# Kernel optimization log

Hardware: AMD Instinct MI355X
Metric: run time of the kernel (lower is better)

Reference implementation:

```python
import jax, jax.numpy as jnp
import numpy as np

# SMPL kinematic tree, first 22 joints (root has parent -1)
PARENTS = [-1, 0, 0, 0, 1, 2, 3, 4, 5, 6, 7, 8, 9, 9, 9, 12, 13, 14, 16, 17, 18, 19]
B, L, J = 64, 2048, 22


def axis_angle_to_matrix(aa):
    """aa: (..., 3) axis-angle -> (..., 3, 3) rotation matrix (Rodrigues)."""
    sq = jnp.sum(aa * aa, axis=-1, keepdims=True)
    angle = jnp.sqrt(sq + 1e-12)
    axis = aa / angle
    x, y, z = axis[..., 0], axis[..., 1], axis[..., 2]
    ang = angle[..., 0]
    c, s = jnp.cos(ang), jnp.sin(ang)
    t = 1.0 - c
    R = jnp.stack([
        t * x * x + c,     t * x * y - s * z, t * x * z + s * y,
        t * x * y + s * z, t * y * y + c,     t * y * z - s * x,
        t * x * z - s * y, t * y * z + s * x, t * z * z + c,
    ], axis=-1)
    return R.reshape(aa.shape[:-1] + (3, 3))


def get_TRS(rotmat, pos):
    """rotmat (...,3,3), pos (...,3) -> homogeneous (...,4,4)."""
    top = jnp.concatenate([rotmat, pos[..., :, None]], axis=-1)  # (...,3,4)
    bottom = jnp.broadcast_to(
        jnp.array([0.0, 0.0, 0.0, 1.0], rotmat.dtype), top.shape[:-2] + (1, 4))
    return jnp.concatenate([top, bottom], axis=-2)


def forward_kinematics(mat, parents):
    """mat: (B,L,J,4,4) local transforms -> global transforms via parent chain."""
    out = [mat[:, :, 0]]
    for j in range(1, mat.shape[2]):
        out.append(out[parents[j]] @ mat[:, :, j])
    return jnp.stack(out, axis=2)


def setup_inputs() -> dict:
    key = jax.random.key(0)
    ks = jax.random.split(key, 6)
    return {
        "body_pose": 0.3 * jax.random.normal(ks[0], (B, L, 63), jnp.float32),
        "betas": jax.random.normal(ks[1], (B, L, 10), jnp.float32),
        "global_orient": 0.3 * jax.random.normal(ks[2], (B, L, 3), jnp.float32),
        "transl": jax.random.normal(ks[3], (B, L, 3), jnp.float32),
        "J_template": jax.random.normal(ks[4], (J, 3), jnp.float32),
        "J_shapedirs": 0.01 * jax.random.normal(ks[5], (J, 3, 10), jnp.float32),
    }


def reference(body_pose, betas, global_orient, transl, J_template, J_shapedirs):
    Bm, Lm = body_pose.shape[:2]
    # (B,L,22,3) axis-angle: global orient + 21 body joints
    aa = jnp.concatenate([global_orient, body_pose], axis=-1).reshape(Bm, Lm, -1, 3)
    rotmat = axis_angle_to_matrix(aa)                                  # (B,L,22,3,3)
    skeleton = J_template[None, None] + jnp.einsum('blk,jck->bljc', betas, J_shapedirs)
    # local offsets: child - parent, root keeps its own position (+ transl)
    parent_idx = jnp.array([0] + PARENTS[1:])
    local = skeleton - skeleton[:, :, parent_idx]
    local = local.at[:, :, 0].set(skeleton[:, :, 0] + transl)
    mat = get_TRS(rotmat, local)                                       # (B,L,22,4,4)
    fk_mat = forward_kinematics(mat, PARENTS)                          # (B,L,22,4,4)
    joints = fk_mat[..., :3, 3]                                        # (B,L,22,3)
    return joints
```

## Files before the change

### kernel.cpp

```cpp
#include <hip/hip_runtime.h>

#define NT  128
#define WSZ 64
#define NJ  22

struct X9 { float r[9]; float t[3]; };

__device__ __forceinline__ void rodrigues(float ax, float ay, float az, float* R) {
    float sq   = ax*ax + ay*ay + az*az + 1e-12f;
    float rinv = rsqrtf(sq);
    float ang  = sq * rinv;
    float s, c;
    __sincosf(ang, &s, &c);
    float x = ax*rinv, y = ay*rinv, z = az*rinv;
    float t = 1.0f - c;
    R[0] = t*x*x + c;   R[1] = t*x*y - s*z; R[2] = t*x*z + s*y;
    R[3] = t*x*y + s*z; R[4] = t*y*y + c;   R[5] = t*y*z - s*x;
    R[6] = t*x*z - s*y; R[7] = t*y*z + s*x; R[8] = t*z*z + c;
}

__device__ __forceinline__ void local_pos(int j, const float* bt,
                                          const float4* LD4, float* lt) {
    #pragma unroll
    for (int c = 0; c < 3; ++c) {
        const float4 a0 = LD4[(j*3 + c)*3 + 0];
        const float4 a1 = LD4[(j*3 + c)*3 + 1];
        const float4 a2 = LD4[(j*3 + c)*3 + 2];
        float v = a2.z;
        v = fmaf(bt[0], a0.x, v); v = fmaf(bt[1], a0.y, v);
        v = fmaf(bt[2], a0.z, v); v = fmaf(bt[3], a0.w, v);
        v = fmaf(bt[4], a1.x, v); v = fmaf(bt[5], a1.y, v);
        v = fmaf(bt[6], a1.z, v); v = fmaf(bt[7], a1.w, v);
        v = fmaf(bt[8], a2.x, v); v = fmaf(bt[9], a2.y, v);
        lt[c] = v;
    }
}

template<int J>
__device__ __forceinline__ X9 step(const X9& gp, const float* aa, const float* bt,
                                   const float4* LD4, float* s_o) {
    float R[9];
    rodrigues(aa[(J-1)*3 + 0], aa[(J-1)*3 + 1], aa[(J-1)*3 + 2], R);
    float lt[3];
    local_pos(J, bt, LD4, lt);
    X9 g;
    #pragma unroll
    for (int r = 0; r < 3; ++r) {
        #pragma unroll
        for (int c = 0; c < 3; ++c)
            g.r[r*3+c] = fmaf(gp.r[r*3+0], R[c],
                         fmaf(gp.r[r*3+1], R[3+c],
                              gp.r[r*3+2] * R[6+c]));
        g.t[r] = fmaf(gp.r[r*3+0], lt[0],
                 fmaf(gp.r[r*3+1], lt[1],
                 fmaf(gp.r[r*3+2], lt[2], gp.t[r])));
    }
    s_o[J*3+0] = g.t[0]; s_o[J*3+1] = g.t[1]; s_o[J*3+2] = g.t[2];
    return g;
}

__global__ __launch_bounds__(NT)
__attribute__((amdgpu_waves_per_eu(2, 2)))
void fk_joints_kernel(
    const float* __restrict__ body_pose,
    const float* __restrict__ betas,
    const float* __restrict__ global_orient,
    const float* __restrict__ transl,
    const float* __restrict__ J_template,
    const float* __restrict__ J_shapedirs,
    float* __restrict__ out)
{
    __shared__ float  s_buf[NT*66];
    __shared__ float4 s_LD4[NJ*3*3];

    const int  tid  = threadIdx.x;
    const int  lane = tid & (WSZ-1);
    const int  wid  = tid >> 6;
    const long long sw = (long long)blockIdx.x * NT + (long long)wid * WSZ;
    const long long s  = sw + lane;

    const float gox = global_orient[s*3 + 0];
    const float goy = global_orient[s*3 + 1];
    const float goz = global_orient[s*3 + 2];
    const float trx = transl[s*3 + 0];
    const float try_ = transl[s*3 + 1];
    const float trz = transl[s*3 + 2];
    float bt[10];
    {
        const float2* b2 = reinterpret_cast<const float2*>(betas + s*10);
        #pragma unroll
        for (int k = 0; k < 5; ++k) {
            float2 v = b2[k];
            bt[2*k+0] = v.x; bt[2*k+1] = v.y;
        }
    }

    float* myb = s_buf + wid * (WSZ*66);
    {
        const float4* src = reinterpret_cast<const float4*>(body_pose + sw*63);
        float4* dst = reinterpret_cast<float4*>(myb);
        #pragma unroll
        for (int i = lane; i < WSZ*63/4; i += WSZ) dst[i] = src[i];
    }

    const int P[NJ] = {0,0,0,0,1,2,3,4,5,6,7,8,9,9,9,12,13,14,16,17,18,19};
    float* s_LD = reinterpret_cast<float*>(s_LD4);
    for (int i = lane; i < NJ*3; i += WSZ) {
        int j = i/3, c = i - j*3;
        float v = J_template[i];
        if (j) v -= J_template[P[j]*3 + c];
        s_LD[i*12 + 10] = v;
        s_LD[i*12 + 11] = 0.0f;
    }
    for (int i = lane; i < NJ*30; i += WSZ) {
        int jc = i/10, k = i - jc*10;
        int j = jc/3,  c = jc - j*3;
        float v = J_shapedirs[i];
        if (j) v -= J_shapedirs[(P[j]*3 + c)*10 + k];
        s_LD[jc*12 + k] = v;
    }
    __builtin_amdgcn_wave_barrier();

    float aa[63];
    #pragma unroll
    for (int k = 0; k < 63; ++k) aa[k] = myb[lane*63 + k];
    __builtin_amdgcn_wave_barrier();

    float* s_o = myb + lane*66;

    X9 g0;
    rodrigues(gox, goy, goz, g0.r);
    {
        float lt0[3];
        local_pos(0, bt, s_LD4, lt0);
        g0.t[0] = lt0[0] + trx;
        g0.t[1] = lt0[1] + try_;
        g0.t[2] = lt0[2] + trz;
        s_o[0] = g0.t[0]; s_o[1] = g0.t[1]; s_o[2] = g0.t[2];
    }

    X9 g;
    g = step<1 >(g0, aa, bt, s_LD4, s_o);
    g = step<4 >(g,  aa, bt, s_LD4, s_o);
    g = step<7 >(g,  aa, bt, s_LD4, s_o);
    g = step<10>(g,  aa, bt, s_LD4, s_o);
    g = step<2 >(g0, aa, bt, s_LD4, s_o);
    g = step<5 >(g,  aa, bt, s_LD4, s_o);
    g = step<8 >(g,  aa, bt, s_LD4, s_o);
    g = step<11>(g,  aa, bt, s_LD4, s_o);
    g = step<3 >(g0, aa, bt, s_LD4, s_o);
    g = step<6 >(g,  aa, bt, s_LD4, s_o);
    X9 g9 = step<9>(g, aa, bt, s_LD4, s_o);
    g = step<12>(g9, aa, bt, s_LD4, s_o);
    g = step<15>(g,  aa, bt, s_LD4, s_o);
    g = step<13>(g9, aa, bt, s_LD4, s_o);
    g = step<16>(g,  aa, bt, s_LD4, s_o);
    g = step<18>(g,  aa, bt, s_LD4, s_o);
    g = step<20>(g,  aa, bt, s_LD4, s_o);
    g = step<14>(g9, aa, bt, s_LD4, s_o);
    g = step<17>(g,  aa, bt, s_LD4, s_o);
    g = step<19>(g,  aa, bt, s_LD4, s_o);
    g = step<21>(g,  aa, bt, s_LD4, s_o);

    __builtin_amdgcn_wave_barrier();

    {
        const float4* src = reinterpret_cast<const float4*>(myb);
        float4* dst = reinterpret_cast<float4*>(out + sw * (NJ*3));
        #pragma unroll
        for (int i = lane; i < WSZ*66/4; i += WSZ) dst[i] = src[i];
    }
}

extern "C" void kernel_launch(void* const* d_in, const int* in_sizes, int n_in,
                              void* d_out, int out_size, void* d_ws, size_t ws_size,
                              hipStream_t stream) {
    const float* body_pose     = (const float*)d_in[0];
    const float* betas         = (const float*)d_in[1];
    const float* global_orient = (const float*)d_in[2];
    const float* transl        = (const float*)d_in[3];
    const float* J_template    = (const float*)d_in[4];
    const float* J_shapedirs   = (const float*)d_in[5];
    float* out = (float*)d_out;

    const int S = in_sizes[0] / 63;
    const int blocks = S / NT;

    hipLaunchKernelGGL(fk_joints_kernel, dim3(blocks), dim3(NT), 0, stream,
                       body_pose, betas, global_orient, transl,
                       J_template, J_shapedirs, out);
}
```

Before: 31.36 us.

## Split each sample's kinematic chain across two lanes for parallel FK

Each wave now processes 32 samples, and two lanes share one sample's kinematic tree. Each lane walks half the joint chains in a fixed 11-step schedule, and joint 9's transform is passed between the pair with shuffles. This halves per-thread register use and serial depth and doubles thread count (256 threads per block, 4 blocks per CU hint). The cost is duplicated root and beta work, extra selects, and a shuffle. Each thread also now loads only 33 pose values instead of 63.

```diff
diff --git a/kernel.cpp b/kernel.cpp
--- a/kernel.cpp
+++ b/kernel.cpp
@@ -1,10 +1,16 @@
 #include <hip/hip_runtime.h>
 
-#define NT  128
-#define WSZ 64
-#define NJ  22
-
-struct X9 { float r[9]; float t[3]; };
+#define NT   256
+#define WSZ  64
+#define SPW  32
+#define NJ   22
+
+__constant__ __device__ const int dummy_unused = 0;
+
+constexpr int cJ0[11] = {3,6,9, 2,5,8,11, 13,16,18,20};
+constexpr int cS0[11] = {1,0,0, 1,0,0,0,  2, 0, 0, 0};
+constexpr int cJ1[11] = {1,4,7,10, 12,15, 14,17,19,21, 12};
+constexpr int cS1[11] = {1,0,0,0,  2, 0,  2, 0, 0, 0,  2};
 
 __device__ __forceinline__ void rodrigues(float ax, float ay, float az, float* R) {
     float sq   = ax*ax + ay*ay + az*az + 1e-12f;
@@ -19,8 +25,8 @@
     R[6] = t*x*z - s*y; R[7] = t*y*z + s*x; R[8] = t*z*z + c;
 }
 
-__device__ __forceinline__ void local_pos(int j, const float* bt,
-                                          const float4* LD4, float* lt) {
+__device__ __forceinline__ void local_pos_rt(int j, const float* bt,
+                                             const float4* LD4, float* lt) {
     #pragma unroll
     for (int c = 0; c < 3; ++c) {
         const float4 a0 = LD4[(j*3 + c)*3 + 0];
@@ -36,32 +42,52 @@
     }
 }
 
-template<int J>
-__device__ __forceinline__ X9 step(const X9& gp, const float* aa, const float* bt,
-                                   const float4* LD4, float* s_o) {
+template<int S>
+__device__ __forceinline__ const float* psel(const float* g, const float* g0, const float* g9s) {
+    if constexpr (S == 0) return g;
+    else if constexpr (S == 1) return g0;
+    else return g9s;
+}
+
+template<int T>
+__device__ __forceinline__ void step2(float* g, const float* g0, const float* g9s,
+                                      int h, const float* aa, const float* bt,
+                                      const float4* LD4, float* s_o ) {
+    constexpr int J0 = cJ0[T], J1 = cJ1[T], S0 = cS0[T], S1 = cS1[T];
+    float gp[12];
+    if constexpr (S0 == S1) {
+        const float* a = psel<S0>(g, g0, g9s);
+        #pragma unroll
+        for (int i = 0; i < 12; ++i) gp[i] = a[i];
+    } else {
+        const float* a = psel<S0>(g, g0, g9s);
+        const float* b = psel<S1>(g, g0, g9s);
+        #pragma unroll
+        for (int i = 0; i < 12; ++i) gp[i] = h ? b[i] : a[i];
+    }
+    const int j = h ? J1 : J0;
     float R[9];
-    rodrigues(aa[(J-1)*3 + 0], aa[(J-1)*3 + 1], aa[(J-1)*3 + 2], R);
+    rodrigues(aa[T*3 + 0], aa[T*3 + 1], aa[T*3 + 2], R);
     float lt[3];
-    local_pos(J, bt, LD4, lt);
-    X9 g;
+    local_pos_rt(j, bt, LD4, lt);
+    float gn[12];
     #pragma unroll
     for (int r = 0; r < 3; ++r) {
         #pragma unroll
         for (int c = 0; c < 3; ++c)
-            g.r[r*3+c] = fmaf(gp.r[r*3+0], R[c],
-                         fmaf(gp.r[r*3+1], R[3+c],
-                              gp.r[r*3+2] * R[6+c]));
-        g.t[r] = fmaf(gp.r[r*3+0], lt[0],
-                 fmaf(gp.r[r*3+1], lt[1],
-                 fmaf(gp.r[r*3+2], lt[2], gp.t[r])));
-    }
-    s_o[J*3+0] = g.t[0]; s_o[J*3+1] = g.t[1]; s_o[J*3+2] = g.t[2];
-    return g;
-}
-
-__global__ __launch_bounds__(NT)
-__attribute__((amdgpu_waves_per_eu(2, 2)))
-void fk_joints_kernel(
+            gn[r*3+c] = fmaf(gp[r*3+0], R[c],
+                        fmaf(gp[r*3+1], R[3+c],
+                             gp[r*3+2] * R[6+c]));
+        gn[9+r] = fmaf(gp[r*3+0], lt[0],
+                  fmaf(gp[r*3+1], lt[1],
+                  fmaf(gp[r*3+2], lt[2], gp[9+r])));
+    }
+    s_o[j*3+0] = gn[9]; s_o[j*3+1] = gn[10]; s_o[j*3+2] = gn[11];
+    #pragma unroll
+    for (int i = 0; i < 12; ++i) g[i] = gn[i];
+}
+
+__global__ __launch_bounds__(NT, 4) void fk_joints_kernel(
     const float* __restrict__ body_pose,
     const float* __restrict__ betas,
     const float* __restrict__ global_orient,
@@ -70,14 +96,16 @@
     const float* __restrict__ J_shapedirs,
     float* __restrict__ out)
 {
-    __shared__ float  s_buf[NT*66];
+    __shared__ float  s_buf[4 * SPW * 66];
     __shared__ float4 s_LD4[NJ*3*3];
 
     const int  tid  = threadIdx.x;
     const int  lane = tid & (WSZ-1);
     const int  wid  = tid >> 6;
-    const long long sw = (long long)blockIdx.x * NT + (long long)wid * WSZ;
-    const long long s  = sw + lane;
+    const int  samp = lane >> 1;
+    const int  h    = lane & 1;
+    const long long sw = (long long)blockIdx.x * (4*SPW) + (long long)wid * SPW;
+    const long long s  = sw + samp;
 
     const float gox = global_orient[s*3 + 0];
     const float goy = global_orient[s*3 + 1];
@@ -95,12 +123,12 @@
         }
     }
 
-    float* myb = s_buf + wid * (WSZ*66);
+    float* myb = s_buf + wid * (SPW*66);
     {
         const float4* src = reinterpret_cast<const float4*>(body_pose + sw*63);
         float4* dst = reinterpret_cast<float4*>(myb);
         #pragma unroll
-        for (int i = lane; i < WSZ*63/4; i += WSZ) dst[i] = src[i];
+        for (int i = lane; i < SPW*63/4; i += WSZ) dst[i] = src[i];
     }
 
     const int P[NJ] = {0,0,0,0,1,2,3,4,5,6,7,8,9,9,9,12,13,14,16,17,18,19};
@@ -121,54 +149,60 @@
     }
     __builtin_amdgcn_wave_barrier();
 
-    float aa[63];
-    #pragma unroll
-    for (int k = 0; k < 63; ++k) aa[k] = myb[lane*63 + k];
+    float aa[33];
+    {
+        const float* mypose = myb + samp*63;
+        #pragma unroll
+        for (int t = 0; t < 11; ++t) {
+            const int off = (h ? (cJ1[t]-1) : (cJ0[t]-1)) * 3;
+            aa[t*3+0] = mypose[off+0];
+            aa[t*3+1] = mypose[off+1];
+            aa[t*3+2] = mypose[off+2];
+        }
+    }
+
+    float g0[12];
+    rodrigues(gox, goy, goz, g0);
+    {
+        float lt0[3];
+        local_pos_rt(0, bt, s_LD4, lt0);
+        g0[9]  = lt0[0] + trx;
+        g0[10] = lt0[1] + try_;
+        g0[11] = lt0[2] + trz;
+    }
     __builtin_amdgcn_wave_barrier();
 
-    float* s_o = myb + lane*66;
-
-    X9 g0;
-    rodrigues(gox, goy, goz, g0.r);
-    {
-        float lt0[3];
-        local_pos(0, bt, s_LD4, lt0);
-        g0.t[0] = lt0[0] + trx;
-        g0.t[1] = lt0[1] + try_;
-        g0.t[2] = lt0[2] + trz;
-        s_o[0] = g0.t[0]; s_o[1] = g0.t[1]; s_o[2] = g0.t[2];
-    }
-
-    X9 g;
-    g = step<1 >(g0, aa, bt, s_LD4, s_o);
-    g = step<4 >(g,  aa, bt, s_LD4, s_o);
-    g = step<7 >(g,  aa, bt, s_LD4, s_o);
-    g = step<10>(g,  aa, bt, s_LD4, s_o);
-    g = step<2 >(g0, aa, bt, s_LD4, s_o);
-    g = step<5 >(g,  aa, bt, s_LD4, s_o);
-    g = step<8 >(g,  aa, bt, s_LD4, s_o);
-    g = step<11>(g,  aa, bt, s_LD4, s_o);
-    g = step<3 >(g0, aa, bt, s_LD4, s_o);
-    g = step<6 >(g,  aa, bt, s_LD4, s_o);
-    X9 g9 = step<9>(g, aa, bt, s_LD4, s_o);
-    g = step<12>(g9, aa, bt, s_LD4, s_o);
-    g = step<15>(g,  aa, bt, s_LD4, s_o);
-    g = step<13>(g9, aa, bt, s_LD4, s_o);
-    g = step<16>(g,  aa, bt, s_LD4, s_o);
-    g = step<18>(g,  aa, bt, s_LD4, s_o);
-    g = step<20>(g,  aa, bt, s_LD4, s_o);
-    g = step<14>(g9, aa, bt, s_LD4, s_o);
-    g = step<17>(g,  aa, bt, s_LD4, s_o);
-    g = step<19>(g,  aa, bt, s_LD4, s_o);
-    g = step<21>(g,  aa, bt, s_LD4, s_o);
+    float* s_o = myb + samp*66;
+    s_o[0] = g0[9]; s_o[1] = g0[10]; s_o[2] = g0[11];
+
+    float g[12];
+    float g9s[12];
+    #pragma unroll
+    for (int i = 0; i < 12; ++i) g9s[i] = 0.0f;
+
+    step2<0>(g, g0, g9s, h, aa, bt, s_LD4, s_o);
+    step2<1>(g, g0, g9s, h, aa, bt, s_LD4, s_o);
+    step2<2>(g, g0, g9s, h, aa, bt, s_LD4, s_o);
+    {
+        const int pairlane = lane & ~1;
+        #pragma unroll
+        for (int i = 0; i < 12; ++i) g9s[i] = __shfl(g[i], pairlane, WSZ);
+    }
+    step2<3>(g, g0, g9s, h, aa, bt, s_LD4, s_o);
+    step2<4>(g, g0, g9s, h, aa, bt, s_LD4, s_o);
+    step2<5>(g, g0, g9s, h, aa, bt, s_LD4, s_o);
+    step2<6>(g, g0, g9s, h, aa, bt, s_LD4, s_o);
+    step2<7>(g, g0, g9s, h, aa, bt, s_LD4, s_o);
+    step2<8>(g, g0, g9s, h, aa, bt, s_LD4, s_o);
+    step2<9>(g, g0, g9s, h, aa, bt, s_LD4, s_o);
+    step2<10>(g, g0, g9s, h, aa, bt, s_LD4, s_o);
 
     __builtin_amdgcn_wave_barrier();
 
     {
         const float4* src = reinterpret_cast<const float4*>(myb);
         float4* dst = reinterpret_cast<float4*>(out + sw * (NJ*3));
-        #pragma unroll
-        for (int i = lane; i < WSZ*66/4; i += WSZ) dst[i] = src[i];
+        for (int i = lane; i < SPW*66/4; i += WSZ) dst[i] = src[i];
     }
 }
 
@@ -184,7 +218,7 @@
     float* out = (float*)d_out;
 
     const int S = in_sizes[0] / 63;
-    const int blocks = S / NT;
+    const int blocks = S / (4*SPW);
 
     hipLaunchKernelGGL(fk_joints_kernel, dim3(blocks), dim3(NT), 0, stream,
                        body_pose, betas, global_orient, transl,
```

Result: slower. 49.52 us (+57.9%).

## Compute skeleton per thread in registers and reuse pose LDS in place

Applied to the files above, without the earlier changes.

Drops the shared-memory table of parent-differenced shape directions. Each thread now regresses its full 22-joint skeleton from betas directly, reading J_shapedirs and J_template as uniform global loads, then subtracts parent positions. Instead of copying all 63 pose values into registers, each step reads its axis-angle from LDS and overwrites the same slots with the joint position. The root goes to a separate small array, and output is gathered with index arithmetic. It also removes the waves_per_eu attribute and shrinks LDS. The cost is more per-thread FMAs (skeleton regression plus subtraction), many scalar constant loads, and a divide/modulo gather in the store loop.

```diff
diff --git a/kernel.cpp b/kernel.cpp
--- a/kernel.cpp
+++ b/kernel.cpp
@@ -3,6 +3,8 @@
 #define NT  128
 #define WSZ 64
 #define NJ  22
+
+constexpr int PARENT[NJ] = {0,0,0,0,1,2,3,4,5,6,7,8,9,9,9,12,13,14,16,17,18,19};
 
 struct X9 { float r[9]; float t[3]; };
 
@@ -19,30 +21,11 @@
     R[6] = t*x*z - s*y; R[7] = t*y*z + s*x; R[8] = t*z*z + c;
 }
 
-__device__ __forceinline__ void local_pos(int j, const float* bt,
-                                          const float4* LD4, float* lt) {
-    #pragma unroll
-    for (int c = 0; c < 3; ++c) {
-        const float4 a0 = LD4[(j*3 + c)*3 + 0];
-        const float4 a1 = LD4[(j*3 + c)*3 + 1];
-        const float4 a2 = LD4[(j*3 + c)*3 + 2];
-        float v = a2.z;
-        v = fmaf(bt[0], a0.x, v); v = fmaf(bt[1], a0.y, v);
-        v = fmaf(bt[2], a0.z, v); v = fmaf(bt[3], a0.w, v);
-        v = fmaf(bt[4], a1.x, v); v = fmaf(bt[5], a1.y, v);
-        v = fmaf(bt[6], a1.z, v); v = fmaf(bt[7], a1.w, v);
-        v = fmaf(bt[8], a2.x, v); v = fmaf(bt[9], a2.y, v);
-        lt[c] = v;
-    }
-}
-
 template<int J>
-__device__ __forceinline__ X9 step(const X9& gp, const float* aa, const float* bt,
-                                   const float4* LD4, float* s_o) {
+__device__ __forceinline__ X9 step(const X9& gp, float* pp, const float* sk) {
     float R[9];
-    rodrigues(aa[(J-1)*3 + 0], aa[(J-1)*3 + 1], aa[(J-1)*3 + 2], R);
-    float lt[3];
-    local_pos(J, bt, LD4, lt);
+    rodrigues(pp[(J-1)*3 + 0], pp[(J-1)*3 + 1], pp[(J-1)*3 + 2], R);
+    const float l0 = sk[J*3+0], l1 = sk[J*3+1], l2 = sk[J*3+2];
     X9 g;
     #pragma unroll
     for (int r = 0; r < 3; ++r) {
@@ -51,17 +34,15 @@
             g.r[r*3+c] = fmaf(gp.r[r*3+0], R[c],
                          fmaf(gp.r[r*3+1], R[3+c],
                               gp.r[r*3+2] * R[6+c]));
-        g.t[r] = fmaf(gp.r[r*3+0], lt[0],
-                 fmaf(gp.r[r*3+1], lt[1],
-                 fmaf(gp.r[r*3+2], lt[2], gp.t[r])));
+        g.t[r] = fmaf(gp.r[r*3+0], l0,
+                 fmaf(gp.r[r*3+1], l1,
+                 fmaf(gp.r[r*3+2], l2, gp.t[r])));
     }
-    s_o[J*3+0] = g.t[0]; s_o[J*3+1] = g.t[1]; s_o[J*3+2] = g.t[2];
+    pp[(J-1)*3+0] = g.t[0]; pp[(J-1)*3+1] = g.t[1]; pp[(J-1)*3+2] = g.t[2];
     return g;
 }
 
-__global__ __launch_bounds__(NT)
-__attribute__((amdgpu_waves_per_eu(2, 2)))
-void fk_joints_kernel(
+__global__ __launch_bounds__(NT) void fk_joints_kernel(
     const float* __restrict__ body_pose,
     const float* __restrict__ betas,
     const float* __restrict__ global_orient,
@@ -70,14 +51,22 @@
     const float* __restrict__ J_shapedirs,
     float* __restrict__ out)
 {
-    __shared__ float  s_buf[NT*66];
-    __shared__ float4 s_LD4[NJ*3*3];
+    __shared__ float s_buf[NT*63];
+    __shared__ float s_root[NT*3];
 
     const int  tid  = threadIdx.x;
     const int  lane = tid & (WSZ-1);
     const int  wid  = tid >> 6;
     const long long sw = (long long)blockIdx.x * NT + (long long)wid * WSZ;
     const long long s  = sw + lane;
+
+    float* myb = s_buf + wid * (WSZ*63);
+
+    {
+        const float4* src = reinterpret_cast<const float4*>(body_pose + sw*63);
+        float4* dst = reinterpret_cast<float4*>(myb);
+        for (int i = lane; i < WSZ*63/4; i += WSZ) dst[i] = src[i];
+    }
 
     const float gox = global_orient[s*3 + 0];
     const float goy = global_orient[s*3 + 1];
@@ -95,80 +84,75 @@
         }
     }
 
-    float* myb = s_buf + wid * (WSZ*66);
-    {
-        const float4* src = reinterpret_cast<const float4*>(body_pose + sw*63);
-        float4* dst = reinterpret_cast<float4*>(myb);
+    float sk[NJ*3];
+    #pragma unroll
+    for (int j = 0; j < NJ; ++j) {
         #pragma unroll
-        for (int i = lane; i < WSZ*63/4; i += WSZ) dst[i] = src[i];
+        for (int c = 0; c < 3; ++c) {
+            float v = J_template[j*3 + c];
+            #pragma unroll
+            for (int k = 0; k < 10; ++k)
+                v = fmaf(bt[k], J_shapedirs[(j*3 + c)*10 + k], v);
+            sk[j*3 + c] = v;
+        }
     }
-
-    const int P[NJ] = {0,0,0,0,1,2,3,4,5,6,7,8,9,9,9,12,13,14,16,17,18,19};
-    float* s_LD = reinterpret_cast<float*>(s_LD4);
-    for (int i = lane; i < NJ*3; i += WSZ) {
-        int j = i/3, c = i - j*3;
-        float v = J_template[i];
-        if (j) v -= J_template[P[j]*3 + c];
-        s_LD[i*12 + 10] = v;
-        s_LD[i*12 + 11] = 0.0f;
+    #pragma unroll
+    for (int j = NJ-1; j >= 1; --j) {
+        #pragma unroll
+        for (int c = 0; c < 3; ++c) sk[j*3 + c] -= sk[PARENT[j]*3 + c];
     }
-    for (int i = lane; i < NJ*30; i += WSZ) {
-        int jc = i/10, k = i - jc*10;
-        int j = jc/3,  c = jc - j*3;
-        float v = J_shapedirs[i];
-        if (j) v -= J_shapedirs[(P[j]*3 + c)*10 + k];
-        s_LD[jc*12 + k] = v;
-    }
-    __builtin_amdgcn_wave_barrier();
-
-    float aa[63];
-    #pragma unroll
-    for (int k = 0; k < 63; ++k) aa[k] = myb[lane*63 + k];
-    __builtin_amdgcn_wave_barrier();
-
-    float* s_o = myb + lane*66;
 
     X9 g0;
     rodrigues(gox, goy, goz, g0.r);
-    {
-        float lt0[3];
-        local_pos(0, bt, s_LD4, lt0);
-        g0.t[0] = lt0[0] + trx;
-        g0.t[1] = lt0[1] + try_;
-        g0.t[2] = lt0[2] + trz;
-        s_o[0] = g0.t[0]; s_o[1] = g0.t[1]; s_o[2] = g0.t[2];
-    }
+    g0.t[0] = sk[0] + trx;
+    g0.t[1] = sk[1] + try_;
+    g0.t[2] = sk[2] + trz;
+    s_root[tid*3+0] = g0.t[0]; s_root[tid*3+1] = g0.t[1]; s_root[tid*3+2] = g0.t[2];
+
+    __builtin_amdgcn_wave_barrier();
+
+    float* pp = myb + lane*63;
 
     X9 g;
-    g = step<1 >(g0, aa, bt, s_LD4, s_o);
-    g = step<4 >(g,  aa, bt, s_LD4, s_o);
-    g = step<7 >(g,  aa, bt, s_LD4, s_o);
-    g = step<10>(g,  aa, bt, s_LD4, s_o);
-    g = step<2 >(g0, aa, bt, s_LD4, s_o);
-    g = step<5 >(g,  aa, bt, s_LD4, s_o);
-    g = step<8 >(g,  aa, bt, s_LD4, s_o);
-    g = step<11>(g,  aa, bt, s_LD4, s_o);
-    g = step<3 >(g0, aa, bt, s_LD4, s_o);
-    g = step<6 >(g,  aa, bt, s_LD4, s_o);
-    X9 g9 = step<9>(g, aa, bt, s_LD4, s_o);
-    g = step<12>(g9, aa, bt, s_LD4, s_o);
-    g = step<15>(g,  aa, bt, s_LD4, s_o);
-    g = step<13>(g9, aa, bt, s_LD4, s_o);
-    g = step<16>(g,  aa, bt, s_LD4, s_o);
-    g = step<18>(g,  aa, bt, s_LD4, s_o);
-    g = step<20>(g,  aa, bt, s_LD4, s_o);
-    g = step<14>(g9, aa, bt, s_LD4, s_o);
-    g = step<17>(g,  aa, bt, s_LD4, s_o);
-    g = step<19>(g,  aa, bt, s_LD4, s_o);
-    g = step<21>(g,  aa, bt, s_LD4, s_o);
+    g = step<1 >(g0, pp, sk);
+    g = step<4 >(g,  pp, sk);
+    g = step<7 >(g,  pp, sk);
+    g = step<10>(g,  pp, sk);
+    g = step<2 >(g0, pp, sk);
+    g = step<5 >(g,  pp, sk);
+    g = step<8 >(g,  pp, sk);
+    g = step<11>(g,  pp, sk);
+    g = step<3 >(g0, pp, sk);
+    g = step<6 >(g,  pp, sk);
+    X9 g9 = step<9>(g, pp, sk);
+    g = step<12>(g9, pp, sk);
+    g = step<15>(g,  pp, sk);
+    g = step<13>(g9, pp, sk);
+    g = step<16>(g,  pp, sk);
+    g = step<18>(g,  pp, sk);
+    g = step<20>(g,  pp, sk);
+    g = step<14>(g9, pp, sk);
+    g = step<17>(g,  pp, sk);
+    g = step<19>(g,  pp, sk);
+    g = step<21>(g,  pp, sk);
 
     __builtin_amdgcn_wave_barrier();
 
     {
-        const float4* src = reinterpret_cast<const float4*>(myb);
+        const float* s_rootw = s_root + wid * (WSZ*3);
         float4* dst = reinterpret_cast<float4*>(out + sw * (NJ*3));
-        #pragma unroll
-        for (int i = lane; i < WSZ*66/4; i += WSZ) dst[i] = src[i];
+        for (int i = lane; i < WSZ*66/4; i += WSZ) {
+            const int f0 = i*4;
+            float v[4];
+            #pragma unroll
+            for (int q = 0; q < 4; ++q) {
+                int f = f0 + q;
+                int sm = f / 66;
+                int r = f - sm*66;
+                v[q] = (r < 3) ? s_rootw[sm*3 + r] : myb[sm*63 + (r - 3)];
+            }
+            dst[i] = make_float4(v[0], v[1], v[2], v[3]);
+        }
     }
 }
 
```

Result: slower. 44.67 us (median of 2 runs) (+42.4%).

## Replace unrolled FK chain with table-driven loop to cut register pressure

Applied to the files above, without the earlier changes.

Replaces the fully unrolled per-joint template chain, and the 63-float register array of axis-angles, with a runtime loop driven by a constant-memory schedule table. Each step reads its pose from LDS and writes the joint position back in place. The root position goes to a separate LDS array and the output is assembled with per-element index math. Shared memory per block shrinks and the waves_per_eu cap is removed, aiming for lower VGPR use and higher occupancy. The cost is loop overhead, branching on the schedule code, integer divides in the store loop and LDS reads in the critical path.

```diff
diff --git a/kernel.cpp b/kernel.cpp
--- a/kernel.cpp
+++ b/kernel.cpp
@@ -4,7 +4,15 @@
 #define WSZ 64
 #define NJ  22
 
-struct X9 { float r[9]; float t[3]; };
+__constant__ int c_code[21] = {
+    1|(1<<8), 4, 7, 10,
+    2|(1<<8), 5, 8, 11,
+    3|(1<<8), 6, 9,
+    12|(2<<8), 15,
+    13|(2<<8), 16, 18, 20,
+    14|(2<<8), 17, 19, 21
+};
+__constant__ int c_par[NJ] = {0,0,0,0,1,2,3,4,5,6,7,8,9,9,9,12,13,14,16,17,18,19};
 
 __device__ __forceinline__ void rodrigues(float ax, float ay, float az, float* R) {
     float sq   = ax*ax + ay*ay + az*az + 1e-12f;
@@ -19,8 +27,8 @@
     R[6] = t*x*z - s*y; R[7] = t*y*z + s*x; R[8] = t*z*z + c;
 }
 
-__device__ __forceinline__ void local_pos(int j, const float* bt,
-                                          const float4* LD4, float* lt) {
+__device__ __forceinline__ void local_pos_rt(int j, const float* bt,
+                                             const float4* LD4, float* lt) {
     #pragma unroll
     for (int c = 0; c < 3; ++c) {
         const float4 a0 = LD4[(j*3 + c)*3 + 0];
@@ -36,32 +44,7 @@
     }
 }
 
-template<int J>
-__device__ __forceinline__ X9 step(const X9& gp, const float* aa, const float* bt,
-                                   const float4* LD4, float* s_o) {
-    float R[9];
-    rodrigues(aa[(J-1)*3 + 0], aa[(J-1)*3 + 1], aa[(J-1)*3 + 2], R);
-    float lt[3];
-    local_pos(J, bt, LD4, lt);
-    X9 g;
-    #pragma unroll
-    for (int r = 0; r < 3; ++r) {
-        #pragma unroll
-        for (int c = 0; c < 3; ++c)
-            g.r[r*3+c] = fmaf(gp.r[r*3+0], R[c],
-                         fmaf(gp.r[r*3+1], R[3+c],
-                              gp.r[r*3+2] * R[6+c]));
-        g.t[r] = fmaf(gp.r[r*3+0], lt[0],
-                 fmaf(gp.r[r*3+1], lt[1],
-                 fmaf(gp.r[r*3+2], lt[2], gp.t[r])));
-    }
-    s_o[J*3+0] = g.t[0]; s_o[J*3+1] = g.t[1]; s_o[J*3+2] = g.t[2];
-    return g;
-}
-
-__global__ __launch_bounds__(NT)
-__attribute__((amdgpu_waves_per_eu(2, 2)))
-void fk_joints_kernel(
+__global__ __launch_bounds__(NT) void fk_joints_kernel(
     const float* __restrict__ body_pose,
     const float* __restrict__ betas,
     const float* __restrict__ global_orient,
@@ -70,7 +53,8 @@
     const float* __restrict__ J_shapedirs,
     float* __restrict__ out)
 {
-    __shared__ float  s_buf[NT*66];
+    __shared__ float  s_buf[NT*63];
+    __shared__ float  s_root[NT*3];
     __shared__ float4 s_LD4[NJ*3*3];
 
     const int  tid  = threadIdx.x;
@@ -78,6 +62,15 @@
     const int  wid  = tid >> 6;
     const long long sw = (long long)blockIdx.x * NT + (long long)wid * WSZ;
     const long long s  = sw + lane;
+
+    float* myb = s_buf + wid * (WSZ*63);
+
+    {
+        const float4* src = reinterpret_cast<const float4*>(body_pose + sw*63);
+        float4* dst = reinterpret_cast<float4*>(myb);
+        #pragma unroll 1
+        for (int i = lane; i < WSZ*63/4; i += WSZ) dst[i] = src[i];
+    }
 
     const float gox = global_orient[s*3 + 0];
     const float goy = global_orient[s*3 + 1];
@@ -95,80 +88,94 @@
         }
     }
 
-    float* myb = s_buf + wid * (WSZ*66);
-    {
-        const float4* src = reinterpret_cast<const float4*>(body_pose + sw*63);
-        float4* dst = reinterpret_cast<float4*>(myb);
-        #pragma unroll
-        for (int i = lane; i < WSZ*63/4; i += WSZ) dst[i] = src[i];
-    }
-
-    const int P[NJ] = {0,0,0,0,1,2,3,4,5,6,7,8,9,9,9,12,13,14,16,17,18,19};
     float* s_LD = reinterpret_cast<float*>(s_LD4);
+    #pragma unroll 1
     for (int i = lane; i < NJ*3; i += WSZ) {
         int j = i/3, c = i - j*3;
         float v = J_template[i];
-        if (j) v -= J_template[P[j]*3 + c];
+        if (j) v -= J_template[c_par[j]*3 + c];
         s_LD[i*12 + 10] = v;
         s_LD[i*12 + 11] = 0.0f;
     }
+    #pragma unroll 1
     for (int i = lane; i < NJ*30; i += WSZ) {
         int jc = i/10, k = i - jc*10;
         int j = jc/3,  c = jc - j*3;
         float v = J_shapedirs[i];
-        if (j) v -= J_shapedirs[(P[j]*3 + c)*10 + k];
+        if (j) v -= J_shapedirs[(c_par[j]*3 + c)*10 + k];
         s_LD[jc*12 + k] = v;
     }
     __builtin_amdgcn_wave_barrier();
 
-    float aa[63];
-    #pragma unroll
-    for (int k = 0; k < 63; ++k) aa[k] = myb[lane*63 + k];
-    __builtin_amdgcn_wave_barrier();
-
-    float* s_o = myb + lane*66;
-
-    X9 g0;
-    rodrigues(gox, goy, goz, g0.r);
+    float g[12], g0r[12], g9r[12];
+    rodrigues(gox, goy, goz, g0r);
     {
         float lt0[3];
-        local_pos(0, bt, s_LD4, lt0);
-        g0.t[0] = lt0[0] + trx;
-        g0.t[1] = lt0[1] + try_;
-        g0.t[2] = lt0[2] + trz;
-        s_o[0] = g0.t[0]; s_o[1] = g0.t[1]; s_o[2] = g0.t[2];
+        local_pos_rt(0, bt, s_LD4, lt0);
+        g0r[9]  = lt0[0] + trx;
+        g0r[10] = lt0[1] + try_;
+        g0r[11] = lt0[2] + trz;
     }
+    s_root[tid*3+0] = g0r[9]; s_root[tid*3+1] = g0r[10]; s_root[tid*3+2] = g0r[11];
+    #pragma unroll
+    for (int i = 0; i < 12; ++i) { g[i] = g0r[i]; g9r[i] = g0r[i]; }
 
-    X9 g;
-    g = step<1 >(g0, aa, bt, s_LD4, s_o);
-    g = step<4 >(g,  aa, bt, s_LD4, s_o);
-    g = step<7 >(g,  aa, bt, s_LD4, s_o);
-    g = step<10>(g,  aa, bt, s_LD4, s_o);
-    g = step<2 >(g0, aa, bt, s_LD4, s_o);
-    g = step<5 >(g,  aa, bt, s_LD4, s_o);
-    g = step<8 >(g,  aa, bt, s_LD4, s_o);
-    g = step<11>(g,  aa, bt, s_LD4, s_o);
-    g = step<3 >(g0, aa, bt, s_LD4, s_o);
-    g = step<6 >(g,  aa, bt, s_LD4, s_o);
-    X9 g9 = step<9>(g, aa, bt, s_LD4, s_o);
-    g = step<12>(g9, aa, bt, s_LD4, s_o);
-    g = step<15>(g,  aa, bt, s_LD4, s_o);
-    g = step<13>(g9, aa, bt, s_LD4, s_o);
-    g = step<16>(g,  aa, bt, s_LD4, s_o);
-    g = step<18>(g,  aa, bt, s_LD4, s_o);
-    g = step<20>(g,  aa, bt, s_LD4, s_o);
-    g = step<14>(g9, aa, bt, s_LD4, s_o);
-    g = step<17>(g,  aa, bt, s_LD4, s_o);
-    g = step<19>(g,  aa, bt, s_LD4, s_o);
-    g = step<21>(g,  aa, bt, s_LD4, s_o);
-
+    float* pp = myb + lane*63;
+    #pragma unroll 1
+    for (int t = 0; t < 21; ++t) {
+        const int code = c_code[t];
+        const int j    = code & 255;
+        const int src  = code >> 8;
+        if (src == 1) {
+            #pragma unroll
+            for (int i = 0; i < 12; ++i) g[i] = g0r[i];
+        } else if (src == 2) {
+            #pragma unroll
+            for (int i = 0; i < 12; ++i) g[i] = g9r[i];
+        }
+        const int pb = (j-1)*3;
+        float R[9];
+        rodrigues(pp[pb+0], pp[pb+1], pp[pb+2], R);
+        float lt[3];
+        local_pos_rt(j, bt, s_LD4, lt);
+        float gn[12];
+        #pragma unroll
+        for (int r = 0; r < 3; ++r) {
+            #pragma unroll
+            for (int c = 0; c < 3; ++c)
+                gn[r*3+c] = fmaf(g[r*3+0], R[c],
+                            fmaf(g[r*3+1], R[3+c],
+                                 g[r*3+2] * R[6+c]));
+            gn[9+r] = fmaf(g[r*3+0], lt[0],
+                      fmaf(g[r*3+1], lt[1],
+                      fmaf(g[r*3+2], lt[2], g[9+r])));
+        }
+        #pragma unroll
+        for (int i = 0; i < 12; ++i) g[i] = gn[i];
+        pp[pb+0] = g[9]; pp[pb+1] = g[10]; pp[pb+2] = g[11];
+        if (j == 9) {
+            #pragma unroll
+            for (int i = 0; i < 12; ++i) g9r[i] = g[i];
+        }
+    }
     __builtin_amdgcn_wave_barrier();
 
     {
-        const float4* src = reinterpret_cast<const float4*>(myb);
+        const float* s_rootw = s_root + wid * (WSZ*3);
         float4* dst = reinterpret_cast<float4*>(out + sw * (NJ*3));
-        #pragma unroll
-        for (int i = lane; i < WSZ*66/4; i += WSZ) dst[i] = src[i];
+        #pragma unroll 1
+        for (int i = lane; i < WSZ*66/4; i += WSZ) {
+            const int f0 = i*4;
+            float v[4];
+            #pragma unroll
+            for (int q = 0; q < 4; ++q) {
+                int f = f0 + q;
+                int sm = f / 66;
+                int r = f - sm*66;
+                v[q] = (r < 3) ? s_rootw[sm*3 + r] : myb[sm*63 + (r - 3)];
+            }
+            dst[i] = make_float4(v[0], v[1], v[2], v[3]);
+        }
     }
 }
 
```

Measured after the change: 34.12 us. 1.09x slower.
